# Optimization experiments

Hardware: AMD Instinct MI355X
Metric: run time of the kernel (lower is better)

## Reference

```python
import jax, jax.numpy as jnp
import numpy as np

EPS = 1e-8

def setup_inputs() -> dict:
    key = jax.random.key(0)
    ks = jax.random.split(key, 7)
    B, S, H, NH, V = 4, 2048, 1024, 8, 2048
    sc = 1.0 / np.sqrt(H)
    return {
        "hidden": jax.random.normal(ks[0], (B, S, H), jnp.float32),
        "prior_w": jax.random.normal(ks[1], (H, NH), jnp.float32) * sc,
        "prior_b": jnp.zeros((NH,), jnp.float32),
        "latent_w": jax.random.normal(ks[2], (H, NH * H), jnp.float32) * sc,
        "latent_b": jnp.zeros((NH * H,), jnp.float32),
        "output_w": jax.random.normal(ks[3], (H, V), jnp.float32) * sc,
        "output_b": jnp.zeros((V,), jnp.float32),
    }

def reference(hidden, prior_w, prior_b, latent_w, latent_b, output_w, output_b):
    B, S, H = hidden.shape
    NH = prior_w.shape[1]
    # prior: sigmoid then renormalize over heads
    prior = jax.nn.sigmoid(hidden @ prior_w + prior_b)              # [B,S,NH]
    prior = prior / (prior.sum(-1, keepdims=True) + EPS)
    # latent: linear -> [B,S,NH,H] -> tanh
    latent = jnp.tanh((hidden @ latent_w + latent_b).reshape(B, S, NH, H))
    # per-head softmax over vocab, weighted sum over heads
    logits = jnp.einsum('bsnh,hv->bsnv', latent, output_w) + output_b
    probs = jax.nn.softmax(logits, axis=-1)                          # [B,S,NH,V]
    return jnp.einsum('bsn,bsnv->bsv', prior, probs)
```

## Files before the change

kernel.cpp:

```cpp
#include <hip/hip_runtime.h>
#include <hip/hip_bf16.h>
#include <stdint.h>

typedef _Float16 f16;
typedef _Float16 f16x8 __attribute__((ext_vector_type(8)));
typedef _Float16 f16x4 __attribute__((ext_vector_type(4)));
typedef float f32x4 __attribute__((ext_vector_type(4)));

#define T_TOK 8192
#define H_DIM 1024
#define NHEAD 8
#define V_DIM 2048

__device__ __forceinline__ void gload16(const void* g, void* l) {
  __builtin_amdgcn_global_load_lds(
      (const __attribute__((address_space(1))) void*)(uintptr_t)g,
      (__attribute__((address_space(3))) void*)(unsigned)(uintptr_t)l,
      16, 0, 0);
}

__device__ __forceinline__ float fast_tanh(float x) {
  float xc = fminf(fmaxf(x, -12.f), 12.f);
  float e = __expf(2.f * xc);
  return (e - 1.f) / (e + 1.f);
}

__device__ __forceinline__ void stage_half(const f16* __restrict__ gRowBase,
                                           char* ldsHalf, int tid, int sl8,
                                           int Kd) {
  const int srow = tid >> 3;
  char* wuni = ldsHalf + ((tid >> 6) << 10);
  gload16(gRowBase + (size_t)srow * Kd + sl8, wuni);
  gload16(gRowBase + (size_t)(srow + 64) * Kd + sl8, wuni + 8192);
}

template <int TANH, int MAP>
__global__ __launch_bounds__(512, 2) void k_gemm(const f16* __restrict__ A,
                                                 const f16* __restrict__ Bt,
                                                 const float* __restrict__ bias,
                                                 f16* __restrict__ C,
                                                 int M, int N, int K) {
  __shared__ __align__(16) f16 sA[2][16384];
  __shared__ __align__(16) f16 sB[2][16384];
  const int tid = threadIdx.x;
  const int lane = tid & 63;
  const int wid = tid >> 6;
  const int wr = wid >> 2, wc = wid & 3;
  int m0, n0;
  if (MAP == 1) {
    const int id = ((int)blockIdx.z * gridDim.y + blockIdx.y) * 8 + blockIdx.x;
    const int r = id >> 8;
    const int x = id & 7;
    const int j = (id >> 3) & 31;
    const int strip = r * 2 + (x >> 2);
    m0 = (((x & 3) << 2) + (j >> 3)) * 256;
    n0 = strip * 2048 + (j & 7) * 256;
  } else {
    const int id = blockIdx.y * 8 + blockIdx.x;
    const int cpx = gridDim.y;
    const int sw = (id & 7) * cpx + (id >> 3);
    m0 = (sw >> 3) * 256;
    n0 = blockIdx.z * 2048 + (sw & 7) * 256;
  }
  const int NT = K >> 6;
  const int sl8 = ((tid & 7) ^ ((tid >> 3) & 7)) << 3;
  const int lo15 = lane & 15;
  const int offk0 = lo15 * 128 + (((lane >> 4)) ^ (lane & 7)) * 16;
  const int offk1 = lo15 * 128 + ((4 + (lane >> 4)) ^ (lane & 7)) * 16;

  const f16* Ag = A + (size_t)m0 * K;
  const f16* Bg = Bt + (size_t)n0 * K;
  char* sAb = (char*)&sA[0][0];
  char* sBb = (char*)&sB[0][0];

  stage_half(Ag, sAb, tid, sl8, K);
  stage_half(Ag + (size_t)128 * K, sAb + 16384, tid, sl8, K);
  stage_half(Bg, sBb, tid, sl8, K);
  stage_half(Bg + (size_t)128 * K, sBb + 16384, tid, sl8, K);
  stage_half(Bg + 64, sBb + 32768, tid, sl8, K);
  stage_half(Bg + (size_t)128 * K + 64, sBb + 32768 + 16384, tid, sl8, K);
  asm volatile("s_waitcnt vmcnt(4)" ::: "memory");
  __builtin_amdgcn_s_barrier();
  __builtin_amdgcn_sched_barrier(0);

  f32x4 acc[8][4] = {};
  f16x8 af0[4], af1[4], bf[4][2];

#define LDA_SET(dst, base, q)                                                  \
  {                                                                            \
    dst[0] = *(const f16x8*)((base) + wr * 16384 + (2 * (q) + 0) * 2048 + offk0); \
    dst[1] = *(const f16x8*)((base) + wr * 16384 + (2 * (q) + 0) * 2048 + offk1); \
    dst[2] = *(const f16x8*)((base) + wr * 16384 + (2 * (q) + 1) * 2048 + offk0); \
    dst[3] = *(const f16x8*)((base) + wr * 16384 + (2 * (q) + 1) * 2048 + offk1); \
  }
#define LDB(base)                                                              \
  {                                                                            \
    _Pragma("unroll") for (int ni = 0; ni < 4; ++ni) {                         \
      bf[ni][0] = *(const f16x8*)((base) + wc * 8192 + ni * 2048 + offk0);     \
      bf[ni][1] = *(const f16x8*)((base) + wc * 8192 + ni * 2048 + offk1);     \
    }                                                                          \
  }
#define MFMA16(q, S)                                                           \
  {                                                                            \
    __builtin_amdgcn_s_setprio(1);                                             \
    _Pragma("unroll") for (int ni = 0; ni < 4; ++ni) {                         \
      acc[2 * (q) + 0][ni] = __builtin_amdgcn_mfma_f32_16x16x32_f16(           \
          S[0], bf[ni][0], acc[2 * (q) + 0][ni], 0, 0, 0);                     \
      acc[2 * (q) + 0][ni] = __builtin_amdgcn_mfma_f32_16x16x32_f16(           \
          S[1], bf[ni][1], acc[2 * (q) + 0][ni], 0, 0, 0);                     \
      acc[2 * (q) + 1][ni] = __builtin_amdgcn_mfma_f32_16x16x32_f16(           \
          S[2], bf[ni][0], acc[2 * (q) + 1][ni], 0, 0, 0);                     \
      acc[2 * (q) + 1][ni] = __builtin_amdgcn_mfma_f32_16x16x32_f16(           \
          S[3], bf[ni][1], acc[2 * (q) + 1][ni], 0, 0, 0);                     \
    }                                                                          \
    __builtin_amdgcn_s_setprio(0);                                             \
  }

  LDA_SET(af0, sAb, 0);

#define HALF(tt, bc)                                                           \
  {                                                                            \
    const char* cA = sAb + (bc)*32768;                                         \
    const char* cB = sBb + (bc)*32768;                                         \
    char* nA = sAb + ((bc) ^ 1) * 32768;                                       \
    char* nB = sBb + (bc)*32768;                                               \
    const int ktA = ((tt) + 1) << 6, ktB = ((tt) + 2) << 6;                    \
    const bool doA = (tt) + 1 < NT, doB = (tt) + 2 < NT;                       \
                                    \
    if (doA) stage_half(Ag + ktA, nA, tid, sl8, K);                            \
    LDB(cB);                                                                   \
    LDA_SET(af1, cA, 1);                                                       \
    __builtin_amdgcn_sched_barrier(0);                                         \
    MFMA16(0, af0);                                                            \
    __builtin_amdgcn_s_barrier();                                              \
                                                                      \
    if (doA) stage_half(Ag + (size_t)128 * K + ktA, nA + 16384, tid, sl8, K);  \
    LDA_SET(af0, cA, 2);                                                       \
    __builtin_amdgcn_sched_barrier(0);                                         \
    MFMA16(1, af1);                                                            \
    __builtin_amdgcn_s_barrier();                                              \
                                                                      \
    if (doB) stage_half(Bg + ktB, nB, tid, sl8, K);                            \
    LDA_SET(af1, cA, 3);                                                       \
    __builtin_amdgcn_sched_barrier(0);                                         \
    MFMA16(2, af0);                                                            \
    __builtin_amdgcn_s_barrier();                                              \
                  \
    if (doB) stage_half(Bg + (size_t)128 * K + ktB, nB + 16384, tid, sl8, K);  \
    if (doB) {                                                                 \
      asm volatile("s_waitcnt vmcnt(4)" ::: "memory");                         \
    } else {                                                                   \
      asm volatile("s_waitcnt vmcnt(0)" ::: "memory");                         \
    }                                                                          \
    __builtin_amdgcn_s_barrier();                                              \
    __builtin_amdgcn_sched_barrier(0);                                         \
    if (doA) LDA_SET(af0, sAb + ((bc) ^ 1) * 32768, 0);                        \
    __builtin_amdgcn_sched_barrier(0);                                         \
    MFMA16(3, af1);                                                            \
  }

#pragma unroll 1
  for (int T = 0; T < NT; T += 2) {
    HALF(T, 0);
    HALF(T + 1, 1);
  }
#undef HALF
#undef LDA_SET
#undef LDB
#undef MFMA16

  const int crow = m0 + wr * 128 + ((lane >> 4) << 2);
  const int ccol0 = n0 + wc * 64 + lo15;
  float bv[4];
#pragma unroll
  for (int ni = 0; ni < 4; ++ni) bv[ni] = bias[ccol0 + ni * 16];
#pragma unroll
  for (int mi = 0; mi < 8; ++mi) {
#pragma unroll
    for (int r = 0; r < 4; ++r) {
      f16* Crow = C + (size_t)(crow + mi * 16 + r) * N;
#pragma unroll
      for (int ni = 0; ni < 4; ++ni) {
        float v = acc[mi][ni][r] + bv[ni];
        if (TANH) v = fast_tanh(v);
        Crow[ccol0 + ni * 16] = (f16)v;
      }
    }
  }
}

__global__ __launch_bounds__(256) void k_transpose(const float* __restrict__ in,
                                                   f16* __restrict__ out,
                                                   int R, int C) {
  __shared__ f16 tile[64][66];
  const int c0 = blockIdx.x * 64, r0 = blockIdx.y * 64;
  const int tid = threadIdx.x;
  const int tr = tid >> 4;
  const int tc4 = (tid & 15) * 4;
#pragma unroll
  for (int i = 0; i < 4; ++i) {
    const int r = tr + i * 16;
    const float4 v = *(const float4*)&in[(size_t)(r0 + r) * C + c0 + tc4];
    tile[tc4 + 0][r] = (f16)v.x;
    tile[tc4 + 1][r] = (f16)v.y;
    tile[tc4 + 2][r] = (f16)v.z;
    tile[tc4 + 3][r] = (f16)v.w;
  }
  __syncthreads();
  const int oc = tid >> 2;
  const int or4 = (tid & 3) * 16;
#pragma unroll
  for (int i = 0; i < 4; ++i) {
    f16x4 w;
    w[0] = tile[oc][or4 + i * 4 + 0];
    w[1] = tile[oc][or4 + i * 4 + 1];
    w[2] = tile[oc][or4 + i * 4 + 2];
    w[3] = tile[oc][or4 + i * 4 + 3];
    *(f16x4*)&out[(size_t)(c0 + oc) * R + r0 + or4 + i * 4] = w;
  }
}

__global__ __launch_bounds__(256) void k_prior_conv(const float* __restrict__ hidden,
                                                    const float* __restrict__ pw,
                                                    const float* __restrict__ pb,
                                                    float* __restrict__ prior,
                                                    f16* __restrict__ hidden_h) {
  const int wid = threadIdx.x >> 6, lane = threadIdx.x & 63;
  const int t = blockIdx.x * 4 + wid;
  const float* hrow = hidden + (size_t)t * H_DIM;
  f16* orow = hidden_h + (size_t)t * H_DIM;
  float acc[NHEAD] = {0.f, 0.f, 0.f, 0.f, 0.f, 0.f, 0.f, 0.f};
#pragma unroll
  for (int i = 0; i < 4; ++i) {
    const int k = i * 256 + lane * 4;
    const float4 v = *(const float4*)(hrow + k);
    f16x4 o;
    o[0] = (f16)v.x; o[1] = (f16)v.y; o[2] = (f16)v.z; o[3] = (f16)v.w;
    *(f16x4*)(orow + k) = o;
    const float vv[4] = {v.x, v.y, v.z, v.w};
#pragma unroll
    for (int j = 0; j < 4; ++j) {
      const float* wr = pw + (size_t)(k + j) * NHEAD;
#pragma unroll
      for (int h = 0; h < NHEAD; ++h) acc[h] += vv[j] * wr[h];
    }
  }
#pragma unroll
  for (int h = 0; h < NHEAD; ++h) {
#pragma unroll
    for (int off = 32; off >= 1; off >>= 1) acc[h] += __shfl_xor(acc[h], off);
  }
  if (lane == 0) {
    float p[NHEAD], s = 0.f;
#pragma unroll
    for (int h = 0; h < NHEAD; ++h) {
      p[h] = 1.f / (1.f + __expf(-(acc[h] + pb[h])));
      s += p[h];
    }
    float inv = 1.f / (s + 1e-8f);
#pragma unroll
    for (int h = 0; h < NHEAD; ++h) prior[t * NHEAD + h] = p[h] * inv;
  }
}

__global__ __launch_bounds__(256) void k_softmax(const f16* __restrict__ logits,
                                                 const float* __restrict__ prior,
                                                 float* __restrict__ out,
                                                 int t0) {
  __shared__ float redsm[NHEAD * 4];
  const int tl = blockIdx.x;
  const int t = t0 + tl;
  const int tid = threadIdx.x, lane = tid & 63, wid = tid >> 6;
  const f16* base = logits + (size_t)tl * NHEAD * V_DIM + tid * 8;

  f16x8 x[NHEAD];
#pragma unroll
  for (int h = 0; h < NHEAD; ++h) x[h] = *(const f16x8*)(base + h * V_DIM);

  float xv[NHEAD][8];
  float sml[NHEAD];
#pragma unroll
  for (int h = 0; h < NHEAD; ++h) {
    float s = 0.f;
#pragma unroll
    for (int j = 0; j < 8; ++j) {
      xv[h][j] = __expf(fminf((float)x[h][j], 50.f));
      s += xv[h][j];
    }
    sml[h] = s;
  }
#pragma unroll
  for (int h = 0; h < NHEAD; ++h) {
#pragma unroll
    for (int off = 32; off >= 1; off >>= 1) sml[h] += __shfl_xor(sml[h], off);
  }
  if (lane == 0) {
#pragma unroll
    for (int h = 0; h < NHEAD; ++h) redsm[h * 4 + wid] = sml[h];
  }
  __syncthreads();

  float oa[8] = {0.f, 0.f, 0.f, 0.f, 0.f, 0.f, 0.f, 0.f};
#pragma unroll
  for (int h = 0; h < NHEAD; ++h) {
    const float s = redsm[h * 4 + 0] + redsm[h * 4 + 1] + redsm[h * 4 + 2] +
                    redsm[h * 4 + 3];
    const float coef = prior[t * NHEAD + h] / s;
#pragma unroll
    for (int j = 0; j < 8; ++j) oa[j] += coef * xv[h][j];
  }
  float4* op = (float4*)(out + (size_t)t * V_DIM + tid * 8);
  op[0] = make_float4(oa[0], oa[1], oa[2], oa[3]);
  op[1] = make_float4(oa[4], oa[5], oa[6], oa[7]);
}

extern "C" void kernel_launch(void* const* d_in, const int* in_sizes, int n_in,
                              void* d_out, int out_size, void* d_ws, size_t ws_size,
                              hipStream_t stream) {
  const float* hidden   = (const float*)d_in[0];
  const float* prior_w  = (const float*)d_in[1];
  const float* prior_b  = (const float*)d_in[2];
  const float* latent_w = (const float*)d_in[3];
  const float* latent_b = (const float*)d_in[4];
  const float* output_w = (const float*)d_in[5];
  const float* output_b = (const float*)d_in[6];
  float* out = (float*)d_out;

  char* ws = (char*)d_ws;
  size_t off = 0;
  auto alloc = [&](size_t bytes) -> void* {
    void* p = ws + off;
    off += (bytes + 255) & ~(size_t)255;
    return p;
  };
  f16* hidden_h = (f16*)alloc((size_t)T_TOK * H_DIM * 2);
  f16* lw_t     = (f16*)alloc((size_t)NHEAD * H_DIM * H_DIM * 2);
  f16* ow_t     = (f16*)alloc((size_t)V_DIM * H_DIM * 2);
  float* prior  = (float*)alloc((size_t)T_TOK * NHEAD * 4);

  int TC = T_TOK / 2;
  while (TC > 256 &&
         off + (size_t)TC * NHEAD * H_DIM * 2 + 256 +
                 (size_t)TC * NHEAD * V_DIM * 2 >
             ws_size)
    TC >>= 1;
  f16* latent_c = (f16*)alloc((size_t)TC * NHEAD * H_DIM * 2);
  f16* logits_c = (f16*)alloc((size_t)TC * NHEAD * V_DIM * 2);

  k_prior_conv<<<T_TOK / 4, 256, 0, stream>>>(hidden, prior_w, prior_b, prior,
                                              hidden_h);
  k_transpose<<<dim3(NHEAD * H_DIM / 64, H_DIM / 64), 256, 0, stream>>>(
      latent_w, lw_t, H_DIM, NHEAD * H_DIM);
  k_transpose<<<dim3(V_DIM / 64, H_DIM / 64), 256, 0, stream>>>(
      output_w, ow_t, H_DIM, V_DIM);

  const int nchunk = T_TOK / TC;
  for (int s = 0; s < nchunk; ++s) {
    if (TC == 4096) {
      k_gemm<1, 1><<<dim3(8, 16, 4), 512, 0, stream>>>(
          hidden_h + (size_t)s * TC * H_DIM, lw_t, latent_b, latent_c, TC,
          NHEAD * H_DIM, H_DIM);
    } else {
      k_gemm<1, 0><<<dim3(8, TC / 256, 4), 512, 0, stream>>>(
          hidden_h + (size_t)s * TC * H_DIM, lw_t, latent_b, latent_c, TC,
          NHEAD * H_DIM, H_DIM);
    }
    k_gemm<0, 0><<<dim3(8, TC * NHEAD / 256, 1), 512, 0, stream>>>(
        latent_c, ow_t, output_b, logits_c, TC * NHEAD, V_DIM, H_DIM);
    k_softmax<<<TC, 256, 0, stream>>>(logits_c, prior, out, s * TC);
  }
}
```

Measured before the change: 539.0 us.

## Switch GEMM to 32x32x16 MFMA with fragment-native LDS staging layout

Replaces the 16x16x32 MFMA inner kernel with 32x32x16 MFMA instructions, cutting the MFMA instruction count and the number of accumulator tiles per wave. The global-to-LDS staging is rearranged so each lane's 16-byte chunk lands where it is read back linearly as an MFMA fragment, removing the XOR swizzle arithmetic. The epilogue is rewritten for the 32x32 accumulator layout. Risks include LDS bank conflicts from the unswizzled layout and less coalesced global loads, since each lane now reads 16 bytes from a different row.

```diff
diff --git a/kernel.cpp b/kernel.cpp
--- a/kernel.cpp
+++ b/kernel.cpp
@@ -6,6 +6,7 @@
 typedef _Float16 f16x8 __attribute__((ext_vector_type(8)));
 typedef _Float16 f16x4 __attribute__((ext_vector_type(4)));
 typedef float f32x4 __attribute__((ext_vector_type(4)));
+typedef float f32x16 __attribute__((ext_vector_type(16)));
 
 #define T_TOK 8192
 #define H_DIM 1024
@@ -23,15 +24,6 @@
   float xc = fminf(fmaxf(x, -12.f), 12.f);
   float e = __expf(2.f * xc);
   return (e - 1.f) / (e + 1.f);
-}
-
-__device__ __forceinline__ void stage_half(const f16* __restrict__ gRowBase,
-                                           char* ldsHalf, int tid, int sl8,
-                                           int Kd) {
-  const int srow = tid >> 3;
-  char* wuni = ldsHalf + ((tid >> 6) << 10);
-  gload16(gRowBase + (size_t)srow * Kd + sl8, wuni);
-  gload16(gRowBase + (size_t)(srow + 64) * Kd + sl8, wuni + 8192);
 }
 
 template <int TANH, int MAP>
@@ -63,60 +55,86 @@
     n0 = blockIdx.z * 2048 + (sw & 7) * 256;
   }
   const int NT = K >> 6;
-  const int sl8 = ((tid & 7) ^ ((tid >> 3) & 7)) << 3;
-  const int lo15 = lane & 15;
-  const int offk0 = lo15 * 128 + (((lane >> 4)) ^ (lane & 7)) * 16;
-  const int offk1 = lo15 * 128 + ((4 + (lane >> 4)) ^ (lane & 7)) * 16;
+  const int l31 = lane & 31;
+  const int lhi = lane >> 5;
 
   const f16* Ag = A + (size_t)m0 * K;
   const f16* Bg = Bt + (size_t)n0 * K;
   char* sAb = (char*)&sA[0][0];
   char* sBb = (char*)&sB[0][0];
 
-  stage_half(Ag, sAb, tid, sl8, K);
-  stage_half(Ag + (size_t)128 * K, sAb + 16384, tid, sl8, K);
-  stage_half(Bg, sBb, tid, sl8, K);
-  stage_half(Bg + (size_t)128 * K, sBb + 16384, tid, sl8, K);
-  stage_half(Bg + 64, sBb + 32768, tid, sl8, K);
-  stage_half(Bg + (size_t)128 * K + 64, sBb + 32768 + 16384, tid, sl8, K);
+  const f16* pA0 = Ag + (size_t)((wid & 3) * 32 + l31) * K +
+                   ((wid >> 2) * 16 + lhi * 8);
+  const f16* pB0 = Bg + (size_t)((wid & 1) * 32 + l31) * K +
+                   (((wid >> 1) & 3) * 16 + lhi * 8);
+  const size_t a2off = (size_t)128 * K;
+  const size_t b1off = (size_t)64 * K;
+  const int dU0 = wid << 10, dU1 = (wid + 8) << 10, dU2 = (wid + 16) << 10,
+            dU3 = (wid + 24) << 10;
+
+#define STAGE_A01(dst, kt)                                                     \
+  {                                                                            \
+    gload16(pA0 + (kt), (dst) + dU0);                                          \
+    gload16(pA0 + 32 + (kt), (dst) + dU1);                                     \
+  }
+#define STAGE_A23(dst, kt)                                                     \
+  {                                                                            \
+    gload16(pA0 + a2off + (kt), (dst) + dU2);                                  \
+    gload16(pA0 + a2off + 32 + (kt), (dst) + dU3);                             \
+  }
+#define STAGE_B01(dst, kt)                                                     \
+  {                                                                            \
+    gload16(pB0 + (kt), (dst) + dU0);                                          \
+    gload16(pB0 + b1off + (kt), (dst) + dU1);                                  \
+  }
+#define STAGE_B23(dst, kt)                                                     \
+  {                                                                            \
+    gload16(pB0 + 2 * b1off + (kt), (dst) + dU2);                              \
+    gload16(pB0 + 3 * b1off + (kt), (dst) + dU3);                              \
+  }
+
+  f32x16 acc[4][2] = {};
+  f16x8 af0[4], af1[4], bf[2][4];
+
+#define LDA4(dst, base, q)                                                     \
+  {                                                                            \
+    const char* p = (base) + ((wr * 16 + (q)*4) << 10) + lane * 16;            \
+    dst[0] = *(const f16x8*)(p);                                               \
+    dst[1] = *(const f16x8*)(p + 1024);                                        \
+    dst[2] = *(const f16x8*)(p + 2048);                                        \
+    dst[3] = *(const f16x8*)(p + 3072);                                        \
+  }
+#define LDB(base)                                                              \
+  {                                                                            \
+    const char* p = (base) + (wc << 13) + lane * 16;                           \
+    _Pragma("unroll") for (int ks = 0; ks < 4; ++ks) {                         \
+      bf[0][ks] = *(const f16x8*)(p + (ks * 2 + 0) * 1024);                    \
+      bf[1][ks] = *(const f16x8*)(p + (ks * 2 + 1) * 1024);                    \
+    }                                                                          \
+  }
+#define MFMA8(ks, S)                                                           \
+  {                                                                            \
+    __builtin_amdgcn_s_setprio(1);                                             \
+    _Pragma("unroll") for (int mi = 0; mi < 4; ++mi) {                         \
+      _Pragma("unroll") for (int n = 0; n < 2; ++n) {                          \
+        acc[mi][n] = __builtin_amdgcn_mfma_f32_32x32x16_f16(                   \
+            S[mi], bf[n][ks], acc[mi][n], 0, 0, 0);                            \
+      }                                                                        \
+    }                                                                          \
+    __builtin_amdgcn_s_setprio(0);                                             \
+  }
+
+  STAGE_A01(sAb, 0);
+  STAGE_A23(sAb, 0);
+  STAGE_B01(sBb, 0);
+  STAGE_B23(sBb, 0);
+  STAGE_B01(sBb + 32768, 64);
+  STAGE_B23(sBb + 32768, 64);
   asm volatile("s_waitcnt vmcnt(4)" ::: "memory");
   __builtin_amdgcn_s_barrier();
   __builtin_amdgcn_sched_barrier(0);
 
-  f32x4 acc[8][4] = {};
-  f16x8 af0[4], af1[4], bf[4][2];
-
-#define LDA_SET(dst, base, q)                                                  \
-  {                                                                            \
-    dst[0] = *(const f16x8*)((base) + wr * 16384 + (2 * (q) + 0) * 2048 + offk0); \
-    dst[1] = *(const f16x8*)((base) + wr * 16384 + (2 * (q) + 0) * 2048 + offk1); \
-    dst[2] = *(const f16x8*)((base) + wr * 16384 + (2 * (q) + 1) * 2048 + offk0); \
-    dst[3] = *(const f16x8*)((base) + wr * 16384 + (2 * (q) + 1) * 2048 + offk1); \
-  }
-#define LDB(base)                                                              \
-  {                                                                            \
-    _Pragma("unroll") for (int ni = 0; ni < 4; ++ni) {                         \
-      bf[ni][0] = *(const f16x8*)((base) + wc * 8192 + ni * 2048 + offk0);     \
-      bf[ni][1] = *(const f16x8*)((base) + wc * 8192 + ni * 2048 + offk1);     \
-    }                                                                          \
-  }
-#define MFMA16(q, S)                                                           \
-  {                                                                            \
-    __builtin_amdgcn_s_setprio(1);                                             \
-    _Pragma("unroll") for (int ni = 0; ni < 4; ++ni) {                         \
-      acc[2 * (q) + 0][ni] = __builtin_amdgcn_mfma_f32_16x16x32_f16(           \
-          S[0], bf[ni][0], acc[2 * (q) + 0][ni], 0, 0, 0);                     \
-      acc[2 * (q) + 0][ni] = __builtin_amdgcn_mfma_f32_16x16x32_f16(           \
-          S[1], bf[ni][1], acc[2 * (q) + 0][ni], 0, 0, 0);                     \
-      acc[2 * (q) + 1][ni] = __builtin_amdgcn_mfma_f32_16x16x32_f16(           \
-          S[2], bf[ni][0], acc[2 * (q) + 1][ni], 0, 0, 0);                     \
-      acc[2 * (q) + 1][ni] = __builtin_amdgcn_mfma_f32_16x16x32_f16(           \
-          S[3], bf[ni][1], acc[2 * (q) + 1][ni], 0, 0, 0);                     \
-    }                                                                          \
-    __builtin_amdgcn_s_setprio(0);                                             \
-  }
-
-  LDA_SET(af0, sAb, 0);
+  LDA4(af0, sAb, 0);
 
 #define HALF(tt, bc)                                                           \
   {                                                                            \
@@ -126,27 +144,27 @@
     char* nB = sBb + (bc)*32768;                                               \
     const int ktA = ((tt) + 1) << 6, ktB = ((tt) + 2) << 6;                    \
     const bool doA = (tt) + 1 < NT, doB = (tt) + 2 < NT;                       \
-                                    \
-    if (doA) stage_half(Ag + ktA, nA, tid, sl8, K);                            \
+                                                                      \
+    if (doA) STAGE_A01(nA, ktA);                                               \
     LDB(cB);                                                                   \
-    LDA_SET(af1, cA, 1);                                                       \
-    __builtin_amdgcn_sched_barrier(0);                                         \
-    MFMA16(0, af0);                                                            \
+    LDA4(af1, cA, 1);                                                          \
+    __builtin_amdgcn_sched_barrier(0);                                         \
+    MFMA8(0, af0);                                                             \
     __builtin_amdgcn_s_barrier();                                              \
                                                                       \
-    if (doA) stage_half(Ag + (size_t)128 * K + ktA, nA + 16384, tid, sl8, K);  \
-    LDA_SET(af0, cA, 2);                                                       \
-    __builtin_amdgcn_sched_barrier(0);                                         \
-    MFMA16(1, af1);                                                            \
+    if (doA) STAGE_A23(nA, ktA);                                               \
+    LDA4(af0, cA, 2);                                                          \
+    __builtin_amdgcn_sched_barrier(0);                                         \
+    MFMA8(1, af1);                                                             \
     __builtin_amdgcn_s_barrier();                                              \
                                                                       \
-    if (doB) stage_half(Bg + ktB, nB, tid, sl8, K);                            \
-    LDA_SET(af1, cA, 3);                                                       \
-    __builtin_amdgcn_sched_barrier(0);                                         \
-    MFMA16(2, af0);                                                            \
+    if (doB) STAGE_B01(nB, ktB);                                               \
+    LDA4(af1, cA, 3);                                                          \
+    __builtin_amdgcn_sched_barrier(0);                                         \
+    MFMA8(2, af0);                                                             \
     __builtin_amdgcn_s_barrier();                                              \
                   \
-    if (doB) stage_half(Bg + (size_t)128 * K + ktB, nB + 16384, tid, sl8, K);  \
+    if (doB) STAGE_B23(nB, ktB);                                               \
     if (doB) {                                                                 \
       asm volatile("s_waitcnt vmcnt(4)" ::: "memory");                         \
     } else {                                                                   \
@@ -154,9 +172,9 @@
     }                                                                          \
     __builtin_amdgcn_s_barrier();                                              \
     __builtin_amdgcn_sched_barrier(0);                                         \
-    if (doA) LDA_SET(af0, sAb + ((bc) ^ 1) * 32768, 0);                        \
-    __builtin_amdgcn_sched_barrier(0);                                         \
-    MFMA16(3, af1);                                                            \
+    if (doA) LDA4(af0, sAb + ((bc) ^ 1) * 32768, 0);                           \
+    __builtin_amdgcn_sched_barrier(0);                                         \
+    MFMA8(3, af1);                                                             \
   }
 
 #pragma unroll 1
@@ -165,25 +183,32 @@
     HALF(T + 1, 1);
   }
 #undef HALF
-#undef LDA_SET
+#undef LDA4
 #undef LDB
-#undef MFMA16
-
-  const int crow = m0 + wr * 128 + ((lane >> 4) << 2);
-  const int ccol0 = n0 + wc * 64 + lo15;
-  float bv[4];
-#pragma unroll
-  for (int ni = 0; ni < 4; ++ni) bv[ni] = bias[ccol0 + ni * 16];
-#pragma unroll
-  for (int mi = 0; mi < 8; ++mi) {
-#pragma unroll
-    for (int r = 0; r < 4; ++r) {
-      f16* Crow = C + (size_t)(crow + mi * 16 + r) * N;
-#pragma unroll
-      for (int ni = 0; ni < 4; ++ni) {
-        float v = acc[mi][ni][r] + bv[ni];
-        if (TANH) v = fast_tanh(v);
-        Crow[ccol0 + ni * 16] = (f16)v;
+#undef MFMA8
+#undef STAGE_A01
+#undef STAGE_A23
+#undef STAGE_B01
+#undef STAGE_B23
+
+  const int ccol0 = n0 + wc * 64 + l31;
+  float bv[2];
+#pragma unroll
+  for (int n = 0; n < 2; ++n) bv[n] = bias[ccol0 + n * 32];
+#pragma unroll
+  for (int mi = 0; mi < 4; ++mi) {
+#pragma unroll
+    for (int rq = 0; rq < 4; ++rq) {
+#pragma unroll
+      for (int r2 = 0; r2 < 4; ++r2) {
+        const int row = m0 + wr * 128 + mi * 32 + r2 + 8 * rq + 4 * lhi;
+        f16* Crow = C + (size_t)row * N;
+#pragma unroll
+        for (int n = 0; n < 2; ++n) {
+          float v = acc[mi][n][rq * 4 + r2] + bv[n];
+          if (TANH) v = fast_tanh(v);
+          Crow[ccol0 + n * 32] = (f16)v;
+        }
       }
     }
   }
```

Result: slower. 622.4 us (+15.5%).
